# Kernel tuning notes

Measured on AMD Instinct MI355X. Metric: run time of the kernel, lower is better.

The kernel has to match this reference:

```python
import jax, jax.numpy as jnp
import numpy as np

V, E, H = 32000, 128, 128

def setup_inputs() -> dict:
    key = jax.random.key(0)
    ks = jax.random.split(key, 12)
    s = 0.05
    x = jax.random.randint(ks[0], (256, 512), 0, V)
    emb = jax.random.normal(ks[1], (V, E), jnp.float32) * s
    Wi = jax.random.normal(ks[2], (E + H, H), jnp.float32) * s
    bi = jnp.zeros((H,), jnp.float32)
    Wf = jax.random.normal(ks[3], (E + H, H), jnp.float32) * s
    bf = jnp.zeros((H,), jnp.float32)
    Wc = jax.random.normal(ks[4], (E + H, H), jnp.float32) * s
    bc = jnp.zeros((H,), jnp.float32)
    Wo = jax.random.normal(ks[5], (E + H, H), jnp.float32) * s
    bo = jnp.zeros((H,), jnp.float32)
    Wout = jax.random.normal(ks[6], (H, V), jnp.float32) * s
    bout = jnp.zeros((V,), jnp.float32)
    return {"x": x, "emb": emb, "Wi": Wi, "bi": bi, "Wf": Wf, "bf": bf,
            "Wc": Wc, "bc": bc, "Wo": Wo, "bo": bo, "Wout": Wout, "bout": bout}

def reference(x, emb, Wi, bi, Wf, bf, Wc, bc, Wo, bo, Wout, bout):
    B, T = x.shape
    xe = emb[x]                       # [B, T, E] embedding gather
    xe_t = jnp.swapaxes(xe, 0, 1)     # [T, B, E] for scan over time

    def step(carry, e_t):
        h, c = carry
        comb = jnp.concatenate([e_t, h], axis=1)          # [B, E+H]
        f = jax.nn.sigmoid(comb @ Wf + bf)
        i = jax.nn.sigmoid(comb @ Wi + bi)
        o = jax.nn.sigmoid(comb @ Wo + bo)
        c_ = jnp.tanh(comb @ Wc + bc)
        c = f * c + i * c_
        h = o * jnp.tanh(c)
        return (h, c), None

    h0 = jnp.zeros((B, H), xe.dtype)
    c0 = jnp.zeros((B, H), xe.dtype)
    (h, _), _ = jax.lax.scan(step, (h0, c0), xe_t)
    return h @ Wout + bout            # [B, V] logits from final hidden state
```

## Files before the change

### kernel.cpp

```cpp
#include <hip/hip_runtime.h>

constexpr int TT = 512;
constexpr int BB = 256;
constexpr int HH = 128;
constexpr int VV = 32000;

typedef _Float16 h2 __attribute__((ext_vector_type(2)));
typedef _Float16 f16x4 __attribute__((ext_vector_type(4)));
typedef _Float16 f16x8 __attribute__((ext_vector_type(8)));
typedef float f32x4 __attribute__((ext_vector_type(4)));

struct __align__(16) H2x4 { h2 a, b, c, d; };

__device__ __forceinline__ h2 pkrtz(float a, float b) {
  return __builtin_bit_cast(h2, __builtin_amdgcn_cvt_pkrtz(a, b));
}
__device__ __forceinline__ float fexp2(float x) {
  return __builtin_amdgcn_exp2f(x);
}
__device__ __forceinline__ float frcp(float x) {
  return __builtin_amdgcn_rcpf(x);
}
template <int CTRL>
__device__ __forceinline__ float qmov(float v) {
  return __builtin_bit_cast(
      float, __builtin_amdgcn_mov_dpp(__builtin_bit_cast(int, v), CTRL, 0xf,
                                      0xf, true));
}

constexpr float SC_SIG = -1.4426950408889634f;
constexpr float SC_TANH = 2.8853900817779268f;

__global__ __launch_bounds__(256, 4) void prep(
    const float* __restrict__ Wi, const float* __restrict__ bi,
    const float* __restrict__ Wf, const float* __restrict__ bf,
    const float* __restrict__ Wc, const float* __restrict__ bc,
    const float* __restrict__ Wo, const float* __restrict__ bo,
    _Float16* __restrict__ Wct, float* __restrict__ bcat,
    const float* __restrict__ Wout, _Float16* __restrict__ Wt) {
  if (blockIdx.x < 512) {
    const int n = blockIdx.x;
    const int g = n & 3;
    const int u = n >> 2;
    const float* Wg = (g == 0) ? Wi : (g == 1) ? Wf : (g == 2) ? Wc : Wo;
    const float* bg = (g == 0) ? bi : (g == 1) ? bf : (g == 2) ? bc : bo;
    const float sc = (g == 2) ? SC_TANH : SC_SIG;
    const int k = threadIdx.x;
    Wct[(size_t)n * 256 + k] = (_Float16)(Wg[(size_t)k * HH + u] * sc);
    if (k == 0) bcat[n] = bg[u] * sc;
  } else {
    const int v = (blockIdx.x - 512) * 256 + threadIdx.x;
#pragma unroll 1
    for (int kc = 0; kc < 16; ++kc) {
      float f[8];
#pragma unroll
      for (int i = 0; i < 8; ++i) f[i] = Wout[(size_t)(kc * 8 + i) * VV + v];
      H2x4 q;
      q.a = pkrtz(f[0], f[1]);
      q.b = pkrtz(f[2], f[3]);
      q.c = pkrtz(f[4], f[5]);
      q.d = pkrtz(f[6], f[7]);
      *(H2x4*)(Wt + (size_t)v * HH + kc * 8) = q;
    }
  }
}

__global__ __launch_bounds__(512, 2) void lstm_rec(
    const int* __restrict__ x, const float* __restrict__ emb,
    const _Float16* __restrict__ Wct, const float* __restrict__ bcat,
    _Float16* __restrict__ hbf) {
  const int b = blockIdx.x;
  const int tid = threadIdx.x;
  const int w = tid >> 6;
  const int l = tid & 63;
  const int n16 = l & 15;
  const int quad = l >> 4;
  const int g = n16 & 3;
  const int nts = n16 >> 2;
  const int u = 16 * w + 4 * nts + quad;
  const int xcol = 4 * u + g;

  __shared__ int xrow[TT];
  __shared__ __align__(16) _Float16 comb[2][HH];
  __shared__ __align__(16) _Float16 xch[64][516];

  xrow[tid] = x[(size_t)b * TT + tid];
  if (tid < HH) comb[0][tid] = (_Float16)0.f;

  f16x8 wh[4][4];
#pragma unroll
  for (int nt = 0; nt < 4; ++nt)
#pragma unroll
    for (int ks = 0; ks < 4; ++ks)
      wh[nt][ks] = *(const f16x8*)(Wct +
                                   (size_t)(64 * w + nt * 16 + n16) * 256 +
                                   128 + ks * 32 + quad * 8);

  f16x8 wfx[4][4];
  f32x4 biasr[4];
#pragma unroll
  for (int nt = 0; nt < 4; ++nt) {
#pragma unroll
    for (int ks = 0; ks < 4; ++ks)
      wfx[nt][ks] = *(const f16x8*)(Wct +
                                    (size_t)(64 * w + nt * 16 + n16) * 256 +
                                    ks * 32 + quad * 8);
    biasr[nt] = *(const f32x4*)(bcat + 64 * w + nt * 16 + quad * 4);
  }

  const float gam = (g == 2) ? -2.f : 1.f;
  const float del = (g == 2) ? 1.f : 0.f;

  const f32x4 ZR4 = {0.f, 0.f, 0.f, 0.f};

  float cst = 0.f;
  float hv = 0.f;
  int buf = 0;

  __syncthreads();

  for (int c = 0; c < 8; ++c) {
#pragma unroll 2
    for (int tt = 0; tt < 4; ++tt) {
      const int vid = xrow[c * 64 + tt * 16 + n16];
      const float* ep = emb + (size_t)vid * HH + quad * 8;
      f16x8 ef[4];
#pragma unroll
      for (int ks = 0; ks < 4; ++ks) {
        const float4 e0 = *(const float4*)(ep + ks * 32);
        const float4 e1 = *(const float4*)(ep + ks * 32 + 4);
        H2x4 q;
        q.a = pkrtz(e0.x, e0.y);
        q.b = pkrtz(e0.z, e0.w);
        q.c = pkrtz(e1.x, e1.y);
        q.d = pkrtz(e1.z, e1.w);
        ef[ks] = __builtin_bit_cast(f16x8, q);
      }
      f32x4 acc[4];
#pragma unroll
      for (int nt = 0; nt < 4; ++nt)
        acc[nt] = __builtin_amdgcn_mfma_f32_16x16x32_f16(wfx[nt][0], ef[0],
                                                         biasr[nt], 0, 0, 0);
#pragma unroll
      for (int ks = 1; ks < 4; ++ks)
#pragma unroll
        for (int nt = 0; nt < 4; ++nt)
          acc[nt] = __builtin_amdgcn_mfma_f32_16x16x32_f16(wfx[nt][ks], ef[ks],
                                                           acc[nt], 0, 0, 0);
#pragma unroll
      for (int nt = 0; nt < 4; ++nt) {
        _Float16* dst = &xch[tt * 16 + n16][64 * w + nt * 16 + quad * 4];
        *(h2*)dst = pkrtz(acc[nt][0], acc[nt][1]);
        *(h2*)(dst + 2) = pkrtz(acc[nt][2], acc[nt][3]);
      }
    }
    __syncthreads();

#pragma unroll 2
    for (int tl = 0; tl < 64; ++tl) {
      const float xe = (float)xch[tl][xcol];

      const _Float16* cb = comb[buf];
      f16x8 hb[4];
#pragma unroll
      for (int ks = 0; ks < 4; ++ks)
        hb[ks] = *(const f16x8*)(cb + ks * 32 + quad * 8);

      f32x4 acc[4];
#pragma unroll
      for (int nt = 0; nt < 4; ++nt)
        acc[nt] = __builtin_amdgcn_mfma_f32_16x16x32_f16(wh[nt][0], hb[0],
                                                         ZR4, 0, 0, 0);
#pragma unroll
      for (int ks = 1; ks < 4; ++ks)
#pragma unroll
        for (int nt = 0; nt < 4; ++nt)
          acc[nt] = __builtin_amdgcn_mfma_f32_16x16x32_f16(wh[nt][ks], hb[ks],
                                                           acc[nt], 0, 0, 0);

      const bool s4 = (n16 & 4) != 0;
      const bool s8 = (n16 & 8) != 0;
      const f32x4 t01 = s4 ? acc[1] : acc[0];
      const f32x4 t23 = s4 ? acc[3] : acc[2];
      const f32x4 avq = s8 ? t23 : t01;
      const bool s1 = (n16 & 1) != 0;
      const bool s2 = (n16 & 2) != 0;
      const float r01 = s1 ? avq[1] : avq[0];
      const float r23 = s1 ? avq[3] : avq[2];
      const float a = (s2 ? r23 : r01) + xe;

      const float act = gam * frcp(1.f + fexp2(a)) + del;

      const float x1 = qmov<0xB1>(act);
      const float x2 = qmov<0x4E>(act);
      const float x3 = qmov<0x4E>(x1);

      cst = x1 * cst + act * x2;
      const float th = 1.f - 2.f * frcp(1.f + fexp2(cst * SC_TANH));
      hv = x3 * th;

      if (g == 0) comb[buf ^ 1][u] = (_Float16)hv;
      __syncthreads();
      buf ^= 1;
    }
  }
  if (g == 0) hbf[(size_t)b * HH + u] = (_Float16)hv;
}

__global__ __launch_bounds__(256, 4) void lstm_out(
    const _Float16* __restrict__ Wt, const _Float16* __restrict__ hbf,
    const float* __restrict__ bout, float* __restrict__ out) {
  const int tid = threadIdx.x;
  const int wv = tid >> 6;
  const int lane = tid & 63;
  const int vblk = blockIdx.x % 250;
  const int batblk = blockIdx.x / 250;
  const int n16 = lane & 15;
  const int quad = lane >> 4;
  const int vbase = vblk * 128 + wv * 32;
  const int batbase = batblk * 64;

  f32x4 acc[4][2] = {};
#pragma unroll
  for (int ks = 0; ks < 4; ++ks) {
    const int k = ks * 32 + quad * 8;
    f16x8 a[4], bf_[2];
#pragma unroll
    for (int mt = 0; mt < 4; ++mt)
      a[mt] = *(const f16x8*)(hbf + (size_t)(batbase + mt * 16 + n16) * HH + k);
#pragma unroll
    for (int vt = 0; vt < 2; ++vt)
      bf_[vt] = *(const f16x8*)(Wt + (size_t)(vbase + vt * 16 + n16) * HH + k);
#pragma unroll
    for (int mt = 0; mt < 4; ++mt)
#pragma unroll
      for (int vt = 0; vt < 2; ++vt)
        acc[mt][vt] = __builtin_amdgcn_mfma_f32_16x16x32_f16(a[mt], bf_[vt],
                                                             acc[mt][vt], 0, 0, 0);
  }
#pragma unroll
  for (int vt = 0; vt < 2; ++vt) {
    const int v = vbase + vt * 16 + n16;
    const float bv = bout[v];
#pragma unroll
    for (int mt = 0; mt < 4; ++mt) {
#pragma unroll
      for (int r = 0; r < 4; ++r) {
        const int bat = batbase + mt * 16 + quad * 4 + r;
        out[(size_t)bat * VV + v] = acc[mt][vt][r] + bv;
      }
    }
  }
}

extern "C" void kernel_launch(void* const* d_in, const int* in_sizes, int n_in,
                              void* d_out, int out_size, void* d_ws,
                              size_t ws_size, hipStream_t stream) {
  const int* x = (const int*)d_in[0];
  const float* emb = (const float*)d_in[1];
  const float* Wi = (const float*)d_in[2];
  const float* bi = (const float*)d_in[3];
  const float* Wf = (const float*)d_in[4];
  const float* bf = (const float*)d_in[5];
  const float* Wc = (const float*)d_in[6];
  const float* bc = (const float*)d_in[7];
  const float* Wo = (const float*)d_in[8];
  const float* bo = (const float*)d_in[9];
  const float* Wout = (const float*)d_in[10];
  const float* bout = (const float*)d_in[11];
  float* out = (float*)d_out;

  _Float16* Wt = (_Float16*)d_ws;
  _Float16* hbf = Wt + (size_t)VV * HH;
  _Float16* Wct = hbf + (size_t)BB * HH;
  float* bcat = (float*)(Wct + 512 * 256);

  prep<<<512 + VV / 256, 256, 0, stream>>>(Wi, bi, Wf, bf, Wc, bc, Wo, bo,
                                           Wct, bcat, Wout, Wt);
  lstm_rec<<<BB, 512, 0, stream>>>(x, emb, Wct, bcat, hbf);
  lstm_out<<<(VV / 128) * (BB / 64), 256, 0, stream>>>(Wt, hbf, bout, out);
}
```

Measured before the change: 404.8 us.

## Overlap Wout fp16 conversion with recurrence and pre-swizzle operands for MFMA loads

Moves the Wout fp32-to-fp16 transpose out of the prep kernel into extra blocks of the recurrent kernel, so the conversion runs on CUs left idle by the 256 recurrence blocks instead of before them. Both Wt and the final hidden state are now written in a fragment-major layout matching the MFMA operand order, so the output GEMM reads each lane's 16-byte fragment contiguously. The extra blocks could compete for memory bandwidth or delay scheduling of recurrence blocks, and the swizzled layouts must be consistent between producer and consumer.

```diff
diff --git a/kernel.cpp b/kernel.cpp
--- a/kernel.cpp
+++ b/kernel.cpp
@@ -36,41 +36,47 @@
     const float* __restrict__ Wf, const float* __restrict__ bf,
     const float* __restrict__ Wc, const float* __restrict__ bc,
     const float* __restrict__ Wo, const float* __restrict__ bo,
-    _Float16* __restrict__ Wct, float* __restrict__ bcat,
-    const float* __restrict__ Wout, _Float16* __restrict__ Wt) {
-  if (blockIdx.x < 512) {
-    const int n = blockIdx.x;
-    const int g = n & 3;
-    const int u = n >> 2;
-    const float* Wg = (g == 0) ? Wi : (g == 1) ? Wf : (g == 2) ? Wc : Wo;
-    const float* bg = (g == 0) ? bi : (g == 1) ? bf : (g == 2) ? bc : bo;
-    const float sc = (g == 2) ? SC_TANH : SC_SIG;
-    const int k = threadIdx.x;
-    Wct[(size_t)n * 256 + k] = (_Float16)(Wg[(size_t)k * HH + u] * sc);
-    if (k == 0) bcat[n] = bg[u] * sc;
-  } else {
-    const int v = (blockIdx.x - 512) * 256 + threadIdx.x;
-#pragma unroll 1
-    for (int kc = 0; kc < 16; ++kc) {
-      float f[8];
-#pragma unroll
-      for (int i = 0; i < 8; ++i) f[i] = Wout[(size_t)(kc * 8 + i) * VV + v];
-      H2x4 q;
-      q.a = pkrtz(f[0], f[1]);
-      q.b = pkrtz(f[2], f[3]);
-      q.c = pkrtz(f[4], f[5]);
-      q.d = pkrtz(f[6], f[7]);
-      *(H2x4*)(Wt + (size_t)v * HH + kc * 8) = q;
-    }
-  }
+    _Float16* __restrict__ Wct, float* __restrict__ bcat) {
+  const int n = blockIdx.x;
+  const int g = n & 3;
+  const int u = n >> 2;
+  const float* Wg = (g == 0) ? Wi : (g == 1) ? Wf : (g == 2) ? Wc : Wo;
+  const float* bg = (g == 0) ? bi : (g == 1) ? bf : (g == 2) ? bc : bo;
+  const float sc = (g == 2) ? SC_TANH : SC_SIG;
+  const int k = threadIdx.x;
+  Wct[(size_t)n * 256 + k] = (_Float16)(Wg[(size_t)k * HH + u] * sc);
+  if (k == 0) bcat[n] = bg[u] * sc;
 }
 
 __global__ __launch_bounds__(512, 2) void lstm_rec(
     const int* __restrict__ x, const float* __restrict__ emb,
     const _Float16* __restrict__ Wct, const float* __restrict__ bcat,
-    _Float16* __restrict__ hbf) {
+    _Float16* __restrict__ hbf, const float* __restrict__ Wout,
+    _Float16* __restrict__ Wt) {
+  const int tid = threadIdx.x;
+
+  if (blockIdx.x >= BB) {
+    const int v = (blockIdx.x - BB) * 512 + tid;
+    if (v < VV) {
+#pragma unroll 1
+      for (int kc = 0; kc < 16; ++kc) {
+        float f[8];
+#pragma unroll
+        for (int i = 0; i < 8; ++i) f[i] = Wout[(size_t)(kc * 8 + i) * VV + v];
+        H2x4 q;
+        q.a = pkrtz(f[0], f[1]);
+        q.b = pkrtz(f[2], f[3]);
+        q.c = pkrtz(f[4], f[5]);
+        q.d = pkrtz(f[6], f[7]);
+        *(f16x8*)(Wt +
+                  ((size_t)(v >> 4) * 256 + kc * 16 + (v & 15)) * 8) =
+            __builtin_bit_cast(f16x8, q);
+      }
+    }
+    return;
+  }
+
   const int b = blockIdx.x;
-  const int tid = threadIdx.x;
   const int w = tid >> 6;
   const int l = tid & 63;
   const int n16 = l & 15;
@@ -204,7 +210,9 @@
       buf ^= 1;
     }
   }
-  if (g == 0) hbf[(size_t)b * HH + u] = (_Float16)hv;
+  if (g == 0)
+    hbf[((size_t)(b >> 4) * 256 + (u >> 3) * 16 + (b & 15)) * 8 + (u & 7)] =
+        (_Float16)hv;
 }
 
 __global__ __launch_bounds__(256, 4) void lstm_out(
@@ -223,14 +231,17 @@
   f32x4 acc[4][2] = {};
 #pragma unroll
   for (int ks = 0; ks < 4; ++ks) {
-    const int k = ks * 32 + quad * 8;
     f16x8 a[4], bf_[2];
 #pragma unroll
     for (int mt = 0; mt < 4; ++mt)
-      a[mt] = *(const f16x8*)(hbf + (size_t)(batbase + mt * 16 + n16) * HH + k);
+      a[mt] = *(const f16x8*)(hbf +
+                              (((size_t)(batblk * 4 + mt) << 8) + (ks << 6) +
+                               lane) * 8);
 #pragma unroll
     for (int vt = 0; vt < 2; ++vt)
-      bf_[vt] = *(const f16x8*)(Wt + (size_t)(vbase + vt * 16 + n16) * HH + k);
+      bf_[vt] = *(const f16x8*)(Wt +
+                                (((size_t)(vblk * 8 + wv * 2 + vt) << 8) +
+                                 (ks << 6) + lane) * 8);
 #pragma unroll
     for (int mt = 0; mt < 4; ++mt)
 #pragma unroll
@@ -275,8 +286,7 @@
   _Float16* Wct = hbf + (size_t)BB * HH;
   float* bcat = (float*)(Wct + 512 * 256);
 
-  prep<<<512 + VV / 256, 256, 0, stream>>>(Wi, bi, Wf, bf, Wc, bc, Wo, bo,
-                                           Wct, bcat, Wout, Wt);
-  lstm_rec<<<BB, 512, 0, stream>>>(x, emb, Wct, bcat, hbf);
+  prep<<<512, 256, 0, stream>>>(Wi, bi, Wf, bf, Wc, bc, Wo, bo, Wct, bcat);
+  lstm_rec<<<BB + 63, 512, 0, stream>>>(x, emb, Wct, bcat, hbf, Wout, Wt);
   lstm_out<<<(VV / 128) * (BB / 64), 256, 0, stream>>>(Wt, hbf, bout, out);
 }
```

Result: no change. 404.2 us (-0.2%).
